# Optimization experiments

Hardware: AMD Instinct MI355X
Metric: run time of the kernel (lower is better)

Reference implementation:

```python
import jax, jax.numpy as jnp
import numpy as np

BS, T, D, R = 8, 256, 2048, 4
N, K, G, GS, H = 8192, 64, 512, 16, 64
MOD_IN, MOD_OUT = K + 5, K + 2


def setup_inputs() -> dict:
    key = jax.random.key(0)
    ks = jax.random.split(key, 8)
    cc_signals = jax.random.normal(ks[0], (BS, T, D), dtype=jnp.float32)
    mod_w1 = jax.random.normal(ks[1], (G, MOD_IN, H), dtype=jnp.float32) * (2.0 / (MOD_IN + H)) ** 0.5
    mod_b1 = jnp.zeros((G, H), dtype=jnp.float32)
    mod_w2 = jax.random.normal(ks[2], (G, H, MOD_OUT), dtype=jnp.float32) * 0.01
    mod_b2 = jax.random.normal(ks[3], (G, MOD_OUT), dtype=jnp.float32) * 0.01
    conn_indices = jax.random.randint(ks[4], (N, K), 0, N, dtype=jnp.int32)
    conn_indices = jnp.sort(conn_indices, axis=-1)
    pos = jnp.arange(N, dtype=jnp.float32)
    neuron_id = jnp.stack([jnp.sin(pos * (2 * np.pi / N)), jnp.cos(pos * (2 * np.pi / N))], axis=-1)
    V0 = jax.random.normal(ks[5], (BS, N), dtype=jnp.float32) * 0.1
    activation0 = jax.nn.sigmoid(V0)
    hebbian0 = jnp.zeros((BS, N, K), dtype=jnp.float32)
    decay0 = jnp.full((BS, N), 0.9, dtype=jnp.float32)
    threshold0 = jnp.zeros((BS, N), dtype=jnp.float32)
    return {"cc_signals": cc_signals, "mod_w1": mod_w1, "mod_b1": mod_b1,
            "mod_w2": mod_w2, "mod_b2": mod_b2, "conn_indices": conn_indices,
            "neuron_id": neuron_id, "V0": V0, "activation0": activation0,
            "hebbian0": hebbian0, "decay0": decay0, "threshold0": threshold0}


def _modulator(activation, hebbian, decay, threshold, neuron_id, w1, b1, w2, b2):
    # [BS, N, K+5]
    nid = jnp.broadcast_to(neuron_id[None], (BS, N, 2))
    mod_in = jnp.concatenate([activation[..., None], hebbian, decay[..., None],
                              threshold[..., None], nid], axis=-1)
    x = mod_in.reshape(BS, G, GS, MOD_IN)
    hdn = jnp.tanh(jnp.einsum('bgsi,gih->bgsh', x, w1) + b1[None, :, None, :])
    out = jnp.einsum('bgsh,gho->bgso', hdn, w2) + b2[None, :, None, :]
    out = out.reshape(BS, N, MOD_OUT)
    return out[..., :K], jax.nn.sigmoid(out[..., K]), out[..., K + 1]


def reference(cc_signals, mod_w1, mod_b1, mod_w2, mod_b2, conn_indices, neuron_id,
              V0, activation0, hebbian0, decay0, threshold0):
    w_conn, decay, threshold = _modulator(activation0, hebbian0, decay0, threshold0,
                                          neuron_id, mod_w1, mod_b1, mod_w2, mod_b2)
    inject_all = jnp.repeat(cc_signals, R, axis=-1)  # [BS, T, N]

    def step(carry, inj_t):
        V, act, heb = carry
        nbr = act[:, conn_indices]                       # [BS, N, K] gather
        recv = jnp.sum(nbr * w_conn, axis=-1) + inj_t    # [BS, N]
        V = decay * V + (1.0 - decay) * recv
        act = jax.nn.sigmoid(V - threshold)
        heb = heb + act[..., None] * nbr
        return (V, act, heb), act

    heb_init = jnp.zeros((BS, N, K), dtype=V0.dtype)
    (_, _, _), acts = jax.lax.scan(step, (V0, activation0, heb_init),
                                   jnp.swapaxes(inject_all, 0, 1))
    act_all = jnp.swapaxes(acts, 0, 1)                   # [BS, T, N]
    mem_out = act_all.reshape(BS, T, D, R).mean(axis=-1)  # readout
    return mem_out
```

## Files before the change

### kernel.cpp

```cpp
#include <hip/hip_runtime.h>
#include <hip/hip_fp16.h>
#include <cstdint>
#include <cstddef>

#define BS 8
#define TT 256
#define DD 2048
#define NN 8192
#define KK 64
#define GG 512
#define GSZ 16
#define HH 64
#define MIN_ 69
#define MOUT_ 66
#define NSL 32
#define SLN 256

typedef float    f32x4 __attribute__((ext_vector_type(4)));
typedef uint32_t u32x4 __attribute__((ext_vector_type(4)));

__global__ __launch_bounds__(256) void modulator_kernel(
    const float* __restrict__ w1, const float* __restrict__ b1,
    const float* __restrict__ w2, const float* __restrict__ b2,
    const float* __restrict__ act0, const float* __restrict__ heb0,
    const float* __restrict__ dec0, const float* __restrict__ thr0,
    const float* __restrict__ nid,
    float* __restrict__ wconn, float* __restrict__ decayB, float* __restrict__ thrB)
{
  const int g = blockIdx.x, b = blockIdx.y, tid = threadIdx.x;
  __shared__ float xs[GSZ][MIN_];
  __shared__ float hd[GSZ][HH];

  const int nbase = g * GSZ;
  for (int j = tid; j < GSZ * KK; j += 256) {
    int s = j >> 6, k = j & 63;
    xs[s][1 + k] = heb0[((size_t)(b * NN + nbase + s)) * KK + k];
  }
  if (tid < GSZ) {
    int n = nbase + tid;
    xs[tid][0]  = act0[b * NN + n];
    xs[tid][65] = dec0[b * NN + n];
    xs[tid][66] = thr0[b * NN + n];
    xs[tid][67] = nid[2 * n];
    xs[tid][68] = nid[2 * n + 1];
  }
  __syncthreads();

  for (int rep = 0; rep < 4; ++rep) {
    int t2 = tid + rep * 256;
    int s = t2 >> 6, h = t2 & 63;
    float acc = b1[g * HH + h];
    const float* w1g = w1 + (size_t)g * MIN_ * HH + h;
    for (int i = 0; i < MIN_; ++i) acc = fmaf(xs[s][i], w1g[(size_t)i * HH], acc);
    hd[s][h] = tanhf(acc);
  }
  __syncthreads();

  for (int j = tid; j < GSZ * MOUT_; j += 256) {
    int s = j / MOUT_, o = j - s * MOUT_;
    float acc = b2[g * MOUT_ + o];
    const float* w2g = w2 + (size_t)g * HH * MOUT_ + o;
    for (int h = 0; h < HH; ++h) acc = fmaf(hd[s][h], w2g[(size_t)h * MOUT_], acc);
    int gidx = b * NN + nbase + s;
    if (o < KK)       wconn[(size_t)gidx * KK + o] = acc;
    else if (o == KK) decayB[gidx] = 1.f / (1.f + expf(-acc));
    else              thrB[gidx]   = acc;
  }
}

__global__ __launch_bounds__(256, 1) void scan_kernel(
    const float* __restrict__ cc, const int* __restrict__ conn,
    const float* __restrict__ V0, const float* __restrict__ act0,
    const float* __restrict__ wconn, const float* __restrict__ decayB,
    const float* __restrict__ thrB,
    float* __restrict__ out, uint32_t* actbuf)
{
  const int tid = threadIdx.x;
  const int b   = blockIdx.x & 7;
  const int sl  = blockIdx.x >> 3;
  const int n    = sl * SLN + tid;
  const int gidx = b * NN + n;

  __shared__ float alds[NN];

  f32x4 w4[16];
  int   ad[KK];
  {
    const f32x4* wr = reinterpret_cast<const f32x4*>(wconn + (size_t)gidx * KK);
    #pragma unroll
    for (int j = 0; j < 16; ++j) w4[j] = wr[j];
    const int4* ir = reinterpret_cast<const int4*>(conn + (size_t)n * KK);
    #pragma unroll
    for (int j = 0; j < KK / 4; ++j) {
      int4 v = ir[j];
      ad[4*j+0] = v.x; ad[4*j+1] = v.y; ad[4*j+2] = v.z; ad[4*j+3] = v.w;
    }
  }
  float V     = V0[gidx];
  float dec   = decayB[gidx];
  float onemd = 1.f - dec;
  float thr   = thrB[gidx];

  {
    const float4* src = reinterpret_cast<const float4*>(act0 + (size_t)b * NN);
    float4* dst = reinterpret_cast<float4*>(alds);
    #pragma unroll
    for (int j = 0; j < 8; ++j) dst[tid + j * 256] = src[tid + j * 256];
  }
  __syncthreads();

  float inj = cc[((size_t)b * TT) * DD + (n >> 2)];

  for (int t = 0; t < TT; ++t) {
    float s0 = 0.f, s1 = 0.f, s2 = 0.f, s3 = 0.f;
    #pragma unroll
    for (int j = 0; j < 16; ++j) {
      s0 = fmaf(alds[ad[4*j+0]], w4[j].x, s0);
      s1 = fmaf(alds[ad[4*j+1]], w4[j].y, s1);
      s2 = fmaf(alds[ad[4*j+2]], w4[j].z, s2);
      s3 = fmaf(alds[ad[4*j+3]], w4[j].w, s3);
    }
    float recv = (s0 + s1) + (s2 + s3) + inj;
    V = dec * V + onemd * recv;
    float x = V - thr;
    float a = 1.f / (1.f + expf(-x));

    const int pw = t & 1;

    if (t != TT - 1) {
      uint32_t word = ((uint32_t)(t + 1) << 16) |
                      (uint32_t)__half_as_ushort(__float2half_rn(a));
      uint32_t* dst = actbuf + (size_t)pw * (BS * NN) + gidx;
      asm volatile("global_store_dword %0, %1, off sc0 sc1"
                   :: "v"(dst), "v"(word) : "memory");
    }

    float p = a + __shfl_xor(a, 1);
    p = p + __shfl_xor(p, 2);
    if ((tid & 3) == 0)
      out[((size_t)b * TT + t) * DD + sl * 64 + (tid >> 2)] = 0.25f * p;

    if (t == TT - 1) break;

    inj = cc[((size_t)b * TT + t + 1) * DD + (n >> 2)];

    const uint32_t* src = actbuf + (size_t)pw * (BS * NN) + (size_t)b * NN;
    const uint32_t expect = (uint32_t)(t + 1) << 16;
    u32x4 vals[8];
    for (;;) {
      #pragma unroll
      for (int j = 0; j < 8; ++j) {
        const uint32_t* p4 = src + (tid << 2) + (j << 10);
        asm volatile("global_load_dwordx4 %0, %1, off sc0 sc1"
                     : "=v"(vals[j]) : "v"(p4));
      }
      asm volatile("s_waitcnt vmcnt(0)" ::: "memory");
      uint32_t bad = 0;
      #pragma unroll
      for (int j = 0; j < 8; ++j) {
        bad |= (vals[j].x & 0xFFFF0000u) ^ expect;
        bad |= (vals[j].y & 0xFFFF0000u) ^ expect;
        bad |= (vals[j].z & 0xFFFF0000u) ^ expect;
        bad |= (vals[j].w & 0xFFFF0000u) ^ expect;
      }
      if (bad == 0) break;
    }
    {
      const int base = (tid << 2);
      #pragma unroll
      for (int j = 0; j < 8; ++j) {
        int o = base + (j << 10);
        alds[o + 0] = __half2float(__ushort_as_half((unsigned short)(vals[j].x & 0xFFFFu)));
        alds[o + 1] = __half2float(__ushort_as_half((unsigned short)(vals[j].y & 0xFFFFu)));
        alds[o + 2] = __half2float(__ushort_as_half((unsigned short)(vals[j].z & 0xFFFFu)));
        alds[o + 3] = __half2float(__ushort_as_half((unsigned short)(vals[j].w & 0xFFFFu)));
      }
    }
    __syncthreads();
  }
}

extern "C" void kernel_launch(void* const* d_in, const int* in_sizes, int n_in,
                              void* d_out, int out_size, void* d_ws, size_t ws_size,
                              hipStream_t stream)
{
  const float* cc   = (const float*)d_in[0];
  const float* w1   = (const float*)d_in[1];
  const float* b1   = (const float*)d_in[2];
  const float* w2   = (const float*)d_in[3];
  const float* b2   = (const float*)d_in[4];
  const int*   conn = (const int*)d_in[5];
  const float* nid  = (const float*)d_in[6];
  const float* V0   = (const float*)d_in[7];
  const float* act0 = (const float*)d_in[8];
  const float* heb0 = (const float*)d_in[9];
  const float* dec0 = (const float*)d_in[10];
  const float* thr0 = (const float*)d_in[11];
  float* out = (float*)d_out;

  char* ws = (char*)d_ws;
  float*    wconn  = (float*)ws;
  float*    decayB = (float*)(ws + (size_t)BS * NN * KK * 4);
  float*    thrB   = decayB + BS * NN;
  uint32_t* actbuf = (uint32_t*)(thrB + BS * NN);

  hipMemsetAsync(actbuf, 0, 2 * BS * NN * sizeof(uint32_t), stream);

  dim3 gA(GG, BS);
  modulator_kernel<<<gA, 256, 0, stream>>>(w1, b1, w2, b2, act0, heb0, dec0, thr0,
                                           nid, wconn, decayB, thrB);
  scan_kernel<<<dim3(BS * NSL), 256, 0, stream>>>(cc, conn, V0, act0, wconn,
                                                  decayB, thrB, out, actbuf);
}
```

Measured before the change: 920.8 us.

## Add per-wave sentinel flags for scan sync; stage modulator weights in LDS

The scan kernel now has each wave publish a step counter to a small sentinel array. Before the full activation buffer is reloaded, a wave spins on 128 flags, so the expensive 32 KB tagged poll runs once instead of repeatedly while other blocks are still busy. The modulator kernel now loops over all batches inside one block per group and stages w1/w2/b2 in LDS, cutting repeated global weight reads. Gather addresses are pre-scaled to byte offsets to save address arithmetic. The extra flag stores add traffic to every step, and the modulator now launches 8x fewer blocks, which reduces its parallelism.

New measurement: 970.2 us. +5.4%, slower.

```diff
diff --git a/kernel.cpp b/kernel.cpp
--- a/kernel.cpp
+++ b/kernel.cpp
@@ -15,6 +15,7 @@
 #define MOUT_ 66
 #define NSL 32
 #define SLN 256
+#define NSENT 128
 
 typedef float    f32x4 __attribute__((ext_vector_type(4)));
 typedef uint32_t u32x4 __attribute__((ext_vector_type(4)));
@@ -27,44 +28,53 @@
     const float* __restrict__ nid,
     float* __restrict__ wconn, float* __restrict__ decayB, float* __restrict__ thrB)
 {
-  const int g = blockIdx.x, b = blockIdx.y, tid = threadIdx.x;
+  const int g = blockIdx.x, tid = threadIdx.x;
+  __shared__ float w1s[MIN_ * HH];
+  __shared__ float w2s[HH * MOUT_];
+  __shared__ float b2s[MOUT_];
   __shared__ float xs[GSZ][MIN_];
-  __shared__ float hd[GSZ][HH];
-
+  __shared__ float hd[GSZ * HH];
+
+  for (int j = tid; j < MIN_ * HH; j += 256) w1s[j] = w1[(size_t)g * MIN_ * HH + j];
+  for (int j = tid; j < HH * MOUT_; j += 256) w2s[j] = w2[(size_t)g * HH * MOUT_ + j];
+  if (tid < MOUT_) b2s[tid] = b2[g * MOUT_ + tid];
+  const float b1v = b1[g * HH + (tid & 63)];
   const int nbase = g * GSZ;
-  for (int j = tid; j < GSZ * KK; j += 256) {
-    int s = j >> 6, k = j & 63;
-    xs[s][1 + k] = heb0[((size_t)(b * NN + nbase + s)) * KK + k];
-  }
-  if (tid < GSZ) {
-    int n = nbase + tid;
-    xs[tid][0]  = act0[b * NN + n];
-    xs[tid][65] = dec0[b * NN + n];
-    xs[tid][66] = thr0[b * NN + n];
-    xs[tid][67] = nid[2 * n];
-    xs[tid][68] = nid[2 * n + 1];
-  }
-  __syncthreads();
-
-  for (int rep = 0; rep < 4; ++rep) {
-    int t2 = tid + rep * 256;
-    int s = t2 >> 6, h = t2 & 63;
-    float acc = b1[g * HH + h];
-    const float* w1g = w1 + (size_t)g * MIN_ * HH + h;
-    for (int i = 0; i < MIN_; ++i) acc = fmaf(xs[s][i], w1g[(size_t)i * HH], acc);
-    hd[s][h] = tanhf(acc);
-  }
-  __syncthreads();
-
-  for (int j = tid; j < GSZ * MOUT_; j += 256) {
-    int s = j / MOUT_, o = j - s * MOUT_;
-    float acc = b2[g * MOUT_ + o];
-    const float* w2g = w2 + (size_t)g * HH * MOUT_ + o;
-    for (int h = 0; h < HH; ++h) acc = fmaf(hd[s][h], w2g[(size_t)h * MOUT_], acc);
-    int gidx = b * NN + nbase + s;
-    if (o < KK)       wconn[(size_t)gidx * KK + o] = acc;
-    else if (o == KK) decayB[gidx] = 1.f / (1.f + expf(-acc));
-    else              thrB[gidx]   = acc;
+
+  for (int b = 0; b < BS; ++b) {
+    __syncthreads();
+    for (int j = tid; j < GSZ * KK; j += 256) {
+      int s = j >> 6, k = j & 63;
+      xs[s][1 + k] = heb0[((size_t)(b * NN + nbase + s)) * KK + k];
+    }
+    if (tid < GSZ) {
+      int n = nbase + tid;
+      xs[tid][0]  = act0[b * NN + n];
+      xs[tid][65] = dec0[b * NN + n];
+      xs[tid][66] = thr0[b * NN + n];
+      xs[tid][67] = nid[2 * n];
+      xs[tid][68] = nid[2 * n + 1];
+    }
+    __syncthreads();
+
+    #pragma unroll
+    for (int rep = 0; rep < 4; ++rep) {
+      int s = rep * 4 + (tid >> 6), h = tid & 63;
+      float acc = b1v;
+      for (int i = 0; i < MIN_; ++i) acc = fmaf(xs[s][i], w1s[i * HH + h], acc);
+      hd[s * HH + h] = tanhf(acc);
+    }
+    __syncthreads();
+
+    for (int j = tid; j < GSZ * MOUT_; j += 256) {
+      int s = j / MOUT_, o = j - s * MOUT_;
+      float acc = b2s[o];
+      for (int h = 0; h < HH; ++h) acc = fmaf(hd[s * HH + h], w2s[h * MOUT_ + o], acc);
+      int gidx = b * NN + nbase + s;
+      if (o < KK)       wconn[(size_t)gidx * KK + o] = acc;
+      else if (o == KK) decayB[gidx] = 1.f / (1.f + expf(-acc));
+      else              thrB[gidx]   = acc;
+    }
   }
 }
 
@@ -73,9 +83,11 @@
     const float* __restrict__ V0, const float* __restrict__ act0,
     const float* __restrict__ wconn, const float* __restrict__ decayB,
     const float* __restrict__ thrB,
-    float* __restrict__ out, uint32_t* actbuf)
+    float* __restrict__ out, uint32_t* actbuf, uint32_t* sent)
 {
-  const int tid = threadIdx.x;
+  const int tid  = threadIdx.x;
+  const int lane = tid & 63;
+  const int wv   = tid >> 6;
   const int b   = blockIdx.x & 7;
   const int sl  = blockIdx.x >> 3;
   const int n    = sl * SLN + tid;
@@ -93,7 +105,8 @@
     #pragma unroll
     for (int j = 0; j < KK / 4; ++j) {
       int4 v = ir[j];
-      ad[4*j+0] = v.x; ad[4*j+1] = v.y; ad[4*j+2] = v.z; ad[4*j+3] = v.w;
+      ad[4*j+0] = v.x << 2; ad[4*j+1] = v.y << 2;
+      ad[4*j+2] = v.z << 2; ad[4*j+3] = v.w << 2;
     }
   }
   float V     = V0[gidx];
@@ -110,15 +123,16 @@
   __syncthreads();
 
   float inj = cc[((size_t)b * TT) * DD + (n >> 2)];
+  const char* abase = reinterpret_cast<const char*>(alds);
 
   for (int t = 0; t < TT; ++t) {
     float s0 = 0.f, s1 = 0.f, s2 = 0.f, s3 = 0.f;
     #pragma unroll
     for (int j = 0; j < 16; ++j) {
-      s0 = fmaf(alds[ad[4*j+0]], w4[j].x, s0);
-      s1 = fmaf(alds[ad[4*j+1]], w4[j].y, s1);
-      s2 = fmaf(alds[ad[4*j+2]], w4[j].z, s2);
-      s3 = fmaf(alds[ad[4*j+3]], w4[j].w, s3);
+      s0 = fmaf(*reinterpret_cast<const float*>(abase + ad[4*j+0]), w4[j].x, s0);
+      s1 = fmaf(*reinterpret_cast<const float*>(abase + ad[4*j+1]), w4[j].y, s1);
+      s2 = fmaf(*reinterpret_cast<const float*>(abase + ad[4*j+2]), w4[j].z, s2);
+      s3 = fmaf(*reinterpret_cast<const float*>(abase + ad[4*j+3]), w4[j].w, s3);
     }
     float recv = (s0 + s1) + (s2 + s3) + inj;
     V = dec * V + onemd * recv;
@@ -133,6 +147,12 @@
       uint32_t* dst = actbuf + (size_t)pw * (BS * NN) + gidx;
       asm volatile("global_store_dword %0, %1, off sc0 sc1"
                    :: "v"(dst), "v"(word) : "memory");
+      if (lane == 0) {
+        uint32_t* sp = sent + (size_t)(pw * BS + b) * NSENT + sl * 4 + wv;
+        uint32_t tv = (uint32_t)(t + 1);
+        asm volatile("global_store_dword %0, %1, off sc0 sc1"
+                     :: "v"(sp), "v"(tv) : "memory");
+      }
     }
 
     float p = a + __shfl_xor(a, 1);
@@ -143,6 +163,20 @@
     if (t == TT - 1) break;
 
     inj = cc[((size_t)b * TT + t + 1) * DD + (n >> 2)];
+
+    {
+      const uint32_t tgt = (uint32_t)(t + 1);
+      const uint32_t* sp = sent + (size_t)(pw * BS + b) * NSENT;
+      for (;;) {
+        uint32_t v0, v1;
+        asm volatile("global_load_dword %0, %1, off sc0 sc1"
+                     : "=v"(v0) : "v"(sp + lane));
+        asm volatile("global_load_dword %0, %1, off sc0 sc1"
+                     : "=v"(v1) : "v"(sp + 64 + lane));
+        asm volatile("s_waitcnt vmcnt(0)" ::: "memory");
+        if (__all(v0 >= tgt && v1 >= tgt)) break;
+      }
+    }
 
     const uint32_t* src = actbuf + (size_t)pw * (BS * NN) + (size_t)b * NN;
     const uint32_t expect = (uint32_t)(t + 1) << 16;
@@ -203,12 +237,12 @@
   float*    decayB = (float*)(ws + (size_t)BS * NN * KK * 4);
   float*    thrB   = decayB + BS * NN;
   uint32_t* actbuf = (uint32_t*)(thrB + BS * NN);
-
-  hipMemsetAsync(actbuf, 0, 2 * BS * NN * sizeof(uint32_t), stream);
-
-  dim3 gA(GG, BS);
-  modulator_kernel<<<gA, 256, 0, stream>>>(w1, b1, w2, b2, act0, heb0, dec0, thr0,
-                                           nid, wconn, decayB, thrB);
+  uint32_t* sent   = actbuf + 2 * BS * NN;
+
+  hipMemsetAsync(actbuf, 0, (2 * BS * NN + 2 * BS * NSENT) * sizeof(uint32_t), stream);
+
+  modulator_kernel<<<dim3(GG), 256, 0, stream>>>(w1, b1, w2, b2, act0, heb0, dec0,
+                                                 thr0, nid, wconn, decayB, thrB);
   scan_kernel<<<dim3(BS * NSL), 256, 0, stream>>>(cc, conn, V0, act0, wconn,
-                                                  decayB, thrB, out, actbuf);
+                                                  decayB, thrB, out, actbuf, sent);
 }
```
